# Kernel optimization log

Hardware: AMD Instinct MI355X
Metric: run time of the kernel (lower is better)

The kernel has to match this reference:

```python
import jax, jax.numpy as jnp
import numpy as np

N_NODES = 50000
N_EDGES = 1600000
IN_C, HID_C, OUT_C = 256, 256, 10


def setup_inputs() -> dict:
    key = jax.random.key(0)
    ks = jax.random.split(key, 8)
    x = jax.random.normal(ks[0], (N_NODES, IN_C), dtype=jnp.float32)
    edge_index = jax.random.randint(ks[1], (2, N_EDGES), 0, N_NODES, dtype=jnp.int64)
    s1 = 1.0 / np.sqrt(IN_C)
    s2 = 1.0 / np.sqrt(HID_C)
    W1l = jax.random.normal(ks[2], (IN_C, HID_C), dtype=jnp.float32) * s1
    W1r = jax.random.normal(ks[3], (IN_C, HID_C), dtype=jnp.float32) * s1
    b1 = jnp.zeros((HID_C,), dtype=jnp.float32)
    W2l = jax.random.normal(ks[4], (HID_C, OUT_C), dtype=jnp.float32) * s2
    W2r = jax.random.normal(ks[5], (HID_C, OUT_C), dtype=jnp.float32) * s2
    b2 = jnp.zeros((OUT_C,), dtype=jnp.float32)
    return {"x": x, "edge_index": edge_index, "W1l": W1l, "W1r": W1r,
            "b1": b1, "W2l": W2l, "W2r": W2r, "b2": b2}


def _mean_agg(x, src, dst, n):
    # scatter-mean of source features into destination nodes
    summed = jax.ops.segment_sum(x[src], dst, num_segments=n)  # [N, C]
    cnt = jax.ops.segment_sum(jnp.ones_like(dst, dtype=x.dtype), dst, num_segments=n)
    return summed / jnp.maximum(cnt, 1.0)[:, None]


def _sage_conv(x, src, dst, Wl, Wr, b):
    # PyG SAGEConv (mean aggr): lin_l(mean_j x_j) + lin_r(x_i) + bias
    n = x.shape[0]
    agg = _mean_agg(x, src, dst, n)
    return agg @ Wl + x @ Wr + b


def reference(x, edge_index, W1l, W1r, b1, W2l, W2r, b2):
    src = edge_index[0]
    dst = edge_index[1]
    h = _sage_conv(x, src, dst, W1l, W1r, b1)
    h = jax.nn.relu(h)  # dropout skipped: eval mode
    out = _sage_conv(h, src, dst, W2l, W2r, b2)
    return jax.nn.log_softmax(out, axis=1)
```

## Files before the change

kernel.cpp:

```cpp
#include <hip/hip_runtime.h>
#include <hip/hip_bf16.h>

#define N_NODES 50000
#define N_EDGES 1600000
#define IN_C 256
#define HID_C 256
#define OUT_C 10
#define SLOT_CAP 96
#define NBUCKET 196
#define CAP2 56
#define M_TILES 391
#define PART_BLOCKS 391
#define GEMM_BLOCKS 1568
#define PREP_BLOCKS 533

typedef short bf16x8 __attribute__((ext_vector_type(8)));
typedef float f32x4 __attribute__((ext_vector_type(4)));

static __device__ __forceinline__ float b2f(short v) {
    unsigned u = (unsigned)(unsigned short)v << 16;
    return __builtin_bit_cast(float, u);
}
static __device__ __forceinline__ short f2b(float f) {
    __hip_bfloat16 h = __float2bfloat16(f);
    return __builtin_bit_cast(short, h);
}
static __device__ __forceinline__ int4 pack8i(float4 a, float4 b) {
    bf16x8 o;
    o[0] = f2b(a.x); o[1] = f2b(a.y); o[2] = f2b(a.z); o[3] = f2b(a.w);
    o[4] = f2b(b.x); o[5] = f2b(b.y); o[6] = f2b(b.z); o[7] = f2b(b.w);
    return __builtin_bit_cast(int4, o);
}

__global__ void k_prep(const float* __restrict__ W1l, const float* __restrict__ W1r,
                       const float* __restrict__ W2l, const float* __restrict__ W2r,
                       __hip_bfloat16* __restrict__ Wt, float* __restrict__ Wt2f,
                       int* __restrict__ part_done) {
    int bid = blockIdx.x;
    if (bid < 512) {
        int idx = bid * 256 + threadIdx.x;
        int n = idx >> 8, k = idx & 255;
        float v = (n < HID_C) ? W1l[k * HID_C + n] : W1r[k * HID_C + (n - HID_C)];
        Wt[idx] = __float2bfloat16(v);
    } else if (bid < 532) {
        int idx = (bid - 512) * 256 + threadIdx.x;
        int r = idx >> 8, k = idx & 255;
        if (r < OUT_C) Wt2f[r * 256 + k] = W2l[k * OUT_C + r];
        else           Wt2f[(16 + r - OUT_C) * 256 + k] = W2r[k * OUT_C + (r - OUT_C)];
    } else {
        if (threadIdx.x == 0) *part_done = 0;
    }
}

__global__ __launch_bounds__(256) void k_gpb(
        const int* __restrict__ src, const int* __restrict__ dst,
        int* __restrict__ part_done, int* __restrict__ ebuf2,
        unsigned char* __restrict__ cnt2,
        int* __restrict__ cnt, unsigned short* __restrict__ slots,
        const float* __restrict__ X, const __hip_bfloat16* __restrict__ Wt,
        const float* __restrict__ b1,
        __hip_bfloat16* __restrict__ Ab, __hip_bfloat16* __restrict__ Bh) {
    __shared__ short Smem[2 * 128 * 64];
    int tid = threadIdx.x;

    if (blockIdx.x < PART_BLOCKS) {
        int* pos = (int*)Smem;
        int pb = blockIdx.x;
        if (tid < NBUCKET) pos[tid] = 0;
        __syncthreads();

        int4 s[4], d[4];
        bool valid[4];
#pragma unroll
        for (int q = 0; q < 4; ++q) {
            int idx = pb * 1024 + q * 256 + tid;
            valid[q] = (idx < N_EDGES / 4);
            if (valid[q]) {
                s[q] = ((const int4*)src)[idx];
                d[q] = ((const int4*)dst)[idx];
            }
        }
#pragma unroll
        for (int q = 0; q < 4; ++q) {
            if (valid[q]) {
                int ss[4] = { s[q].x, s[q].y, s[q].z, s[q].w };
                int dd[4] = { d[q].x, d[q].y, d[q].z, d[q].w };
#pragma unroll
                for (int e = 0; e < 4; ++e) {
                    int b = dd[e] >> 8;
                    int p = atomicAdd(&pos[b], 1);
                    if (p < CAP2)
                        ebuf2[((size_t)pb * NBUCKET + b) * CAP2 + p] =
                            ss[e] | ((dd[e] & 255) << 16);
                }
            }
        }
        __syncthreads();
        if (tid < NBUCKET) {
            int c = pos[tid];
            cnt2[(size_t)pb * NBUCKET + tid] = (unsigned char)(c > CAP2 ? CAP2 : c);
        }
        __syncthreads();
        if (tid == 0)
            __hip_atomic_fetch_add(part_done, 1, __ATOMIC_RELEASE, __HIP_MEMORY_SCOPE_AGENT);
        return;
    }

    if (blockIdx.x >= PART_BLOCKS + GEMM_BLOCKS) {
        if (tid == 0) {
            while (__hip_atomic_load(part_done, __ATOMIC_RELAXED,
                                     __HIP_MEMORY_SCOPE_AGENT) < PART_BLOCKS)
                __builtin_amdgcn_s_sleep(8);
        }
        __syncthreads();
        asm volatile("" ::: "memory");

        int* lcnt = (int*)Smem;
        int b = blockIdx.x - PART_BLOCKS - GEMM_BLOCKS;
        lcnt[tid] = 0;
        __syncthreads();
        for (int blk = tid; blk < PART_BLOCKS; blk += 256) {
            int len = cnt2[(size_t)blk * NBUCKET + b];
            const int* base2 = ebuf2 + ((size_t)blk * NBUCKET + b) * CAP2;
            for (int i = 0; i < len; ++i) {
                int rec = base2[i];
                int dl = (rec >> 16) & 255;
                int p = atomicAdd(&lcnt[dl], 1);
                if (p < SLOT_CAP)
                    slots[(size_t)(b * 256 + dl) * SLOT_CAP + p] = (unsigned short)(rec & 0xFFFF);
            }
        }
        __syncthreads();
        int nid = b * 256 + tid;
        if (nid < N_NODES) cnt[nid] = lcnt[tid];
        return;
    }

    short* As = Smem;
    short* Bs = Smem + 128 * 64;
    int fid = blockIdx.x - PART_BLOCKS;
    int xcd = fid & 7, slot = fid >> 3;
    int m_t = (slot >> 2) * 8 + xcd;
    if (m_t >= M_TILES) return;
    int n_t = slot & 3;
    int m_base = m_t * 128;
    int n_base = n_t * 128;

    int wave = tid >> 6, lane = tid & 63;
    int r = lane & 15, quad = lane >> 4;
    int wr = wave >> 1, wc = wave & 1;

    int srow = tid >> 3;
    int kb8  = (tid & 7) * 16;
    int kelem = (tid & 7) * 8;
    int swz  = kb8 ^ ((srow & 7) << 4);

    f32x4 acc[4][4];
#pragma unroll
    for (int i = 0; i < 4; ++i)
#pragma unroll
        for (int j = 0; j < 4; ++j) acc[i][j] = f32x4{0.f, 0.f, 0.f, 0.f};

    int4 av[4], bv[4];
#pragma unroll
    for (int q = 0; q < 4; ++q) {
        int grow = m_base + q * 32 + srow;
        if (grow > N_NODES - 1) grow = N_NODES - 1;
        const float* xp = X + (size_t)grow * IN_C + kelem;
        av[q] = pack8i(*(const float4*)xp, *(const float4*)(xp + 4));
        int brow = n_base + q * 32 + srow;
        bv[q] = *(const int4*)((const char*)Wt + ((size_t)brow * 512 + kb8));
    }

    for (int kk = 0; kk < 4; ++kk) {
        if (kk) __syncthreads();
#pragma unroll
        for (int q = 0; q < 4; ++q) {
            *(int4*)((char*)As + (size_t)((q * 32 + srow) * 128 + swz)) = av[q];
            *(int4*)((char*)Bs + (size_t)((q * 32 + srow) * 128 + swz)) = bv[q];
        }
        __syncthreads();

        if (kk < 3) {
            int ke = (kk + 1) * 64 + kelem;
            int kbyte = (kk + 1) * 128 + kb8;
#pragma unroll
            for (int q = 0; q < 4; ++q) {
                int grow = m_base + q * 32 + srow;
                if (grow > N_NODES - 1) grow = N_NODES - 1;
                const float* xp = X + (size_t)grow * IN_C + ke;
                av[q] = pack8i(*(const float4*)xp, *(const float4*)(xp + 4));
                int brow = n_base + q * 32 + srow;
                bv[q] = *(const int4*)((const char*)Wt + ((size_t)brow * 512 + kbyte));
            }
        }

#pragma unroll
        for (int s = 0; s < 2; ++s) {
            int kfb = (s * 64 + quad * 16) ^ ((r & 7) << 4);
            bf16x8 a[4], b[4];
#pragma unroll
            for (int i = 0; i < 4; ++i)
                a[i] = *(const bf16x8*)((const char*)As + (size_t)((wr * 64 + i * 16 + r) * 128) + kfb);
#pragma unroll
            for (int j = 0; j < 4; ++j)
                b[j] = *(const bf16x8*)((const char*)Bs + (size_t)((wc * 64 + j * 16 + r) * 128) + kfb);
#pragma unroll
            for (int i = 0; i < 4; ++i)
#pragma unroll
                for (int j = 0; j < 4; ++j)
                    acc[i][j] = __builtin_amdgcn_mfma_f32_16x16x32_bf16(a[i], b[j], acc[i][j], 0, 0, 0);
        }
    }

    __syncthreads();
    short* Cs = Smem;
    bool left = (n_base < HID_C);
#pragma unroll
    for (int j = 0; j < 4; ++j) {
        int coll = wc * 64 + 16 * j + r;
        float bias = left ? 0.f : b1[n_base + coll - HID_C];
#pragma unroll
        for (int i = 0; i < 4; ++i) {
#pragma unroll
            for (int ii = 0; ii < 4; ++ii) {
                int rowl = wr * 64 + 16 * i + quad * 4 + ii;
                int byteoff = (coll * 2) ^ ((rowl & 7) << 4);
                *(short*)((char*)Cs + rowl * 256 + byteoff) = f2b(acc[i][j][ii] + bias);
            }
        }
    }
    __syncthreads();

    int rrow = tid >> 4;
    int cchunk = (tid & 15) * 16;
    size_t colbyte = left ? (size_t)(n_base * 2) : (size_t)((n_base - HID_C) * 2);
    char* outp = left ? (char*)Ab : (char*)Bh;
    for (int rb = 0; rb < 128; rb += 16) {
        int rowl = rb + rrow;
        int4 v = *(const int4*)((const char*)Cs + rowl * 256 + (cchunk ^ ((rowl & 7) << 4)));
        int grow = m_base + rowl;
        if (grow < N_NODES)
            *(int4*)(outp + (size_t)grow * 512 + colbyte + cchunk) = v;
    }
}

__global__ __launch_bounds__(256) void k_agg1f(
        const __hip_bfloat16* __restrict__ Ab, const __hip_bfloat16* __restrict__ Bh,
        const int* __restrict__ cnt, const unsigned short* __restrict__ slots,
        const float* __restrict__ Wt2f, const float* __restrict__ b2,
        float* __restrict__ CDl, float* __restrict__ CDr) {
    int wave = threadIdx.x >> 6, lane = threadIdx.x & 63;
    int nid = blockIdx.x * 4 + wave;
    int half = lane >> 5;
    int c8 = (lane & 31) * 8;
    const unsigned short* row = slots + (size_t)nid * SLOT_CAP;
    int n = cnt[nid];
    if (n > SLOT_CAP) n = SLOT_CAP;
    int mid = (n + 1) >> 1;
    int beg = half ? mid : 0;
    int end = half ? n : mid;

    float s0[8], s1[8], s2[8], s3[8];
#pragma unroll
    for (int j = 0; j < 8; ++j) { s0[j] = 0.f; s1[j] = 0.f; s2[j] = 0.f; s3[j] = 0.f; }

    const __hip_bfloat16* abc = Ab + c8;
    int e = beg;
    for (; e + 4 <= end; e += 4) {
        int i0 = row[e], i1 = row[e + 1], i2 = row[e + 2], i3 = row[e + 3];
        bf16x8 v0 = *(const bf16x8*)(abc + (size_t)i0 * HID_C);
        bf16x8 v1 = *(const bf16x8*)(abc + (size_t)i1 * HID_C);
        bf16x8 v2 = *(const bf16x8*)(abc + (size_t)i2 * HID_C);
        bf16x8 v3 = *(const bf16x8*)(abc + (size_t)i3 * HID_C);
#pragma unroll
        for (int j = 0; j < 8; ++j) {
            s0[j] += b2f(v0[j]); s1[j] += b2f(v1[j]);
            s2[j] += b2f(v2[j]); s3[j] += b2f(v3[j]);
        }
    }
    for (; e < end; ++e) {
        int i0 = row[e];
        bf16x8 v0 = *(const bf16x8*)(abc + (size_t)i0 * HID_C);
#pragma unroll
        for (int j = 0; j < 8; ++j) s0[j] += b2f(v0[j]);
    }
#pragma unroll
    for (int j = 0; j < 8; ++j) s0[j] += (s1[j] + s2[j]) + s3[j];
#pragma unroll
    for (int j = 0; j < 8; ++j) s0[j] += __shfl_down(s0[j], 32, 64);

    float h[8];
    float inv = 1.f / fmaxf((float)n, 1.f);
    if (half == 0) {
        bf16x8 bb = *(const bf16x8*)(Bh + (size_t)nid * HID_C + c8);
#pragma unroll
        for (int j = 0; j < 8; ++j)
            h[j] = fmaxf(s0[j] * inv + b2f(bb[j]), 0.f);
    }
#pragma unroll
    for (int j = 0; j < 8; ++j) h[j] = __shfl(h[j], lane & 31, 64);

    const float* wbase = Wt2f + (half ? 16 * 256 : 0);
    float acc[10];
#pragma unroll
    for (int j = 0; j < 10; ++j) {
        f32x4 w0 = *(const f32x4*)(wbase + j * 256 + c8);
        f32x4 w1 = *(const f32x4*)(wbase + j * 256 + c8 + 4);
        float a = h[0] * w0[0] + h[1] * w0[1] + h[2] * w0[2] + h[3] * w0[3]
                + h[4] * w1[0] + h[5] * w1[1] + h[6] * w1[2] + h[7] * w1[3];
#pragma unroll
        for (int off = 16; off > 0; off >>= 1)
            a += __shfl_down(a, off, 32);
        acc[j] = a;
    }
    if ((lane & 31) == 0) {
        if (half == 0) {
            float* o = CDl + (size_t)nid * 12;
#pragma unroll
            for (int j = 0; j < 10; ++j) o[j] = acc[j];
            o[10] = 0.f; o[11] = 0.f;
        } else {
            float* o = CDr + (size_t)nid * 12;
#pragma unroll
            for (int j = 0; j < 10; ++j) o[j] = acc[j] + b2[j];
        }
    }
}

__global__ __launch_bounds__(256) void k_agg2(
        const float* __restrict__ CDl, const float* __restrict__ CDr,
        const int* __restrict__ cnt, const unsigned short* __restrict__ slots,
        float* __restrict__ out) {
    int wave = threadIdx.x >> 6, lane = threadIdx.x & 63;
    int half = lane >> 5, sub = lane & 31;
    int nid = blockIdx.x * 8 + wave * 2 + half;
    const unsigned short* row = slots + (size_t)nid * SLOT_CAP;
    int n = cnt[nid];
    if (n > SLOT_CAP) n = SLOT_CAP;
    float s[10];
#pragma unroll
    for (int j = 0; j < 10; ++j) s[j] = 0.f;
    for (int e = sub; e < n; e += 32) {
        const float* cr = CDl + (size_t)row[e] * 12;
        f32x4 v0 = *(const f32x4*)cr;
        f32x4 v1 = *(const f32x4*)(cr + 4);
        f32x4 v2 = *(const f32x4*)(cr + 8);
#pragma unroll
        for (int j = 0; j < 4; ++j) { s[j] += v0[j]; s[4 + j] += v1[j]; }
        s[8] += v2[0]; s[9] += v2[1];
    }
#pragma unroll
    for (int j = 0; j < 10; ++j)
#pragma unroll
        for (int off = 16; off > 0; off >>= 1)
            s[j] += __shfl_down(s[j], off, 32);
    if (sub == 0) {
        float inv = 1.f / fmaxf((float)n, 1.f);
        const float* rr = CDr + (size_t)nid * 12;
        float z[10], mx = -1e30f;
#pragma unroll
        for (int j = 0; j < 10; ++j) {
            z[j] = s[j] * inv + rr[j];
            mx = fmaxf(mx, z[j]);
        }
        float se = 0.f;
#pragma unroll
        for (int j = 0; j < 10; ++j) se += expf(z[j] - mx);
        float lse = logf(se) + mx;
#pragma unroll
        for (int j = 0; j < 10; ++j) out[(size_t)nid * OUT_C + j] = z[j] - lse;
    }
}

extern "C" void kernel_launch(void* const* d_in, const int* in_sizes, int n_in,
                              void* d_out, int out_size, void* d_ws, size_t ws_size,
                              hipStream_t stream) {
    const float* x   = (const float*)d_in[0];
    const int*   ei  = (const int*)d_in[1];
    const float* W1l = (const float*)d_in[2];
    const float* W1r = (const float*)d_in[3];
    const float* b1  = (const float*)d_in[4];
    const float* W2l = (const float*)d_in[5];
    const float* W2r = (const float*)d_in[6];
    const float* b2  = (const float*)d_in[7];
    float* out = (float*)d_out;
    const int* src = ei;
    const int* dst = ei + N_EDGES;

    char* w = (char*)d_ws;
    size_t off = 0;
    auto alloc = [&](size_t bytes) -> void* {
        void* p = w + off;
        off = (off + bytes + 255) & ~(size_t)255;
        return p;
    };
    __hip_bfloat16* Wt   = (__hip_bfloat16*)alloc((size_t)2 * HID_C * IN_C * 2);
    float*          Wt2f = (float*)alloc((size_t)32 * 256 * 4);
    __hip_bfloat16* Ab   = (__hip_bfloat16*)alloc((size_t)N_NODES * HID_C * 2);
    __hip_bfloat16* Bh   = (__hip_bfloat16*)alloc((size_t)N_NODES * HID_C * 2);
    float* CDl = (float*)alloc((size_t)N_NODES * 12 * 4);
    float* CDr = (float*)alloc((size_t)N_NODES * 12 * 4);
    int* cnt      = (int*)alloc((size_t)N_NODES * 4);
    unsigned short* slots = (unsigned short*)alloc((size_t)N_NODES * SLOT_CAP * 2);
    int* part_done = (int*)alloc(4);
    int* ebuf2     = (int*)alloc((size_t)PART_BLOCKS * NBUCKET * CAP2 * 4);
    unsigned char* cnt2 = (unsigned char*)alloc((size_t)PART_BLOCKS * NBUCKET);

    k_prep<<<PREP_BLOCKS, 256, 0, stream>>>(W1l, W1r, W2l, W2r, Wt, Wt2f, part_done);
    k_gpb<<<PART_BLOCKS + GEMM_BLOCKS + NBUCKET, 256, 0, stream>>>(
        src, dst, part_done, ebuf2, cnt2, cnt, slots, x, Wt, b1, Ab, Bh);
    k_agg1f<<<N_NODES / 4, 256, 0, stream>>>(Ab, Bh, cnt, slots, Wt2f, b2, CDl, CDr);
    k_agg2<<<N_NODES / 8, 256, 0, stream>>>(CDl, CDr, cnt, slots, out);
}
```

Baseline: 339.6 us.

## Move edge partitioning into prep kernel and drop spin-wait flag

Edge partitioning moves from the fused GEMM/bucket kernel into the weight-prep kernel. Bucket-fill blocks now run first in the second kernel and no longer spin-wait on an atomic completion counter, because the kernel boundary orders them after partitioning. This removes the spin-wait and the flag reset. The cost is that partitioning no longer overlaps with the layer-1 GEMM blocks, so partition work sits on the critical path before the GEMM starts.

Result: faster. 320.2 us (-5.7%).

```diff
diff --git a/kernel.cpp b/kernel.cpp
--- a/kernel.cpp
+++ b/kernel.cpp
@@ -12,7 +12,7 @@
 #define M_TILES 391
 #define PART_BLOCKS 391
 #define GEMM_BLOCKS 1568
-#define PREP_BLOCKS 533
+#define PREP_BLOCKS 532
 
 typedef short bf16x8 __attribute__((ext_vector_type(8)));
 typedef float f32x4 __attribute__((ext_vector_type(4)));
@@ -32,30 +32,70 @@
     return __builtin_bit_cast(int4, o);
 }
 
-__global__ void k_prep(const float* __restrict__ W1l, const float* __restrict__ W1r,
-                       const float* __restrict__ W2l, const float* __restrict__ W2r,
-                       __hip_bfloat16* __restrict__ Wt, float* __restrict__ Wt2f,
-                       int* __restrict__ part_done) {
+__global__ __launch_bounds__(256) void k_pp(
+        const float* __restrict__ W1l, const float* __restrict__ W1r,
+        const float* __restrict__ W2l, const float* __restrict__ W2r,
+        __hip_bfloat16* __restrict__ Wt, float* __restrict__ Wt2f,
+        const int* __restrict__ src, const int* __restrict__ dst,
+        int* __restrict__ ebuf2, unsigned char* __restrict__ cnt2) {
+    __shared__ int pos[NBUCKET];
+    int tid = threadIdx.x;
     int bid = blockIdx.x;
+
     if (bid < 512) {
-        int idx = bid * 256 + threadIdx.x;
+        int idx = bid * 256 + tid;
         int n = idx >> 8, k = idx & 255;
         float v = (n < HID_C) ? W1l[k * HID_C + n] : W1r[k * HID_C + (n - HID_C)];
         Wt[idx] = __float2bfloat16(v);
-    } else if (bid < 532) {
-        int idx = (bid - 512) * 256 + threadIdx.x;
+        return;
+    }
+    if (bid < PREP_BLOCKS) {
+        int idx = (bid - 512) * 256 + tid;
         int r = idx >> 8, k = idx & 255;
         if (r < OUT_C) Wt2f[r * 256 + k] = W2l[k * OUT_C + r];
         else           Wt2f[(16 + r - OUT_C) * 256 + k] = W2r[k * OUT_C + (r - OUT_C)];
-    } else {
-        if (threadIdx.x == 0) *part_done = 0;
-    }
-}
-
-__global__ __launch_bounds__(256) void k_gpb(
-        const int* __restrict__ src, const int* __restrict__ dst,
-        int* __restrict__ part_done, int* __restrict__ ebuf2,
-        unsigned char* __restrict__ cnt2,
+        return;
+    }
+
+    int pb = bid - PREP_BLOCKS;
+    if (tid < NBUCKET) pos[tid] = 0;
+    __syncthreads();
+
+    int4 s[4], d[4];
+    bool valid[4];
+#pragma unroll
+    for (int q = 0; q < 4; ++q) {
+        int idx = pb * 1024 + q * 256 + tid;
+        valid[q] = (idx < N_EDGES / 4);
+        if (valid[q]) {
+            s[q] = ((const int4*)src)[idx];
+            d[q] = ((const int4*)dst)[idx];
+        }
+    }
+#pragma unroll
+    for (int q = 0; q < 4; ++q) {
+        if (valid[q]) {
+            int ss[4] = { s[q].x, s[q].y, s[q].z, s[q].w };
+            int dd[4] = { d[q].x, d[q].y, d[q].z, d[q].w };
+#pragma unroll
+            for (int e = 0; e < 4; ++e) {
+                int b = dd[e] >> 8;
+                int p = atomicAdd(&pos[b], 1);
+                if (p < CAP2)
+                    ebuf2[((size_t)pb * NBUCKET + b) * CAP2 + p] =
+                        ss[e] | ((dd[e] & 255) << 16);
+            }
+        }
+    }
+    __syncthreads();
+    if (tid < NBUCKET) {
+        int c = pos[tid];
+        cnt2[(size_t)pb * NBUCKET + tid] = (unsigned char)(c > CAP2 ? CAP2 : c);
+    }
+}
+
+__global__ __launch_bounds__(256) void k_gb(
+        const int* __restrict__ ebuf2, const unsigned char* __restrict__ cnt2,
         int* __restrict__ cnt, unsigned short* __restrict__ slots,
         const float* __restrict__ X, const __hip_bfloat16* __restrict__ Wt,
         const float* __restrict__ b1,
@@ -63,60 +103,9 @@
     __shared__ short Smem[2 * 128 * 64];
     int tid = threadIdx.x;
 
-    if (blockIdx.x < PART_BLOCKS) {
-        int* pos = (int*)Smem;
-        int pb = blockIdx.x;
-        if (tid < NBUCKET) pos[tid] = 0;
-        __syncthreads();
-
-        int4 s[4], d[4];
-        bool valid[4];
-#pragma unroll
-        for (int q = 0; q < 4; ++q) {
-            int idx = pb * 1024 + q * 256 + tid;
-            valid[q] = (idx < N_EDGES / 4);
-            if (valid[q]) {
-                s[q] = ((const int4*)src)[idx];
-                d[q] = ((const int4*)dst)[idx];
-            }
-        }
-#pragma unroll
-        for (int q = 0; q < 4; ++q) {
-            if (valid[q]) {
-                int ss[4] = { s[q].x, s[q].y, s[q].z, s[q].w };
-                int dd[4] = { d[q].x, d[q].y, d[q].z, d[q].w };
-#pragma unroll
-                for (int e = 0; e < 4; ++e) {
-                    int b = dd[e] >> 8;
-                    int p = atomicAdd(&pos[b], 1);
-                    if (p < CAP2)
-                        ebuf2[((size_t)pb * NBUCKET + b) * CAP2 + p] =
-                            ss[e] | ((dd[e] & 255) << 16);
-                }
-            }
-        }
-        __syncthreads();
-        if (tid < NBUCKET) {
-            int c = pos[tid];
-            cnt2[(size_t)pb * NBUCKET + tid] = (unsigned char)(c > CAP2 ? CAP2 : c);
-        }
-        __syncthreads();
-        if (tid == 0)
-            __hip_atomic_fetch_add(part_done, 1, __ATOMIC_RELEASE, __HIP_MEMORY_SCOPE_AGENT);
-        return;
-    }
-
-    if (blockIdx.x >= PART_BLOCKS + GEMM_BLOCKS) {
-        if (tid == 0) {
-            while (__hip_atomic_load(part_done, __ATOMIC_RELAXED,
-                                     __HIP_MEMORY_SCOPE_AGENT) < PART_BLOCKS)
-                __builtin_amdgcn_s_sleep(8);
-        }
-        __syncthreads();
-        asm volatile("" ::: "memory");
-
+    if (blockIdx.x < NBUCKET) {
         int* lcnt = (int*)Smem;
-        int b = blockIdx.x - PART_BLOCKS - GEMM_BLOCKS;
+        int b = blockIdx.x;
         lcnt[tid] = 0;
         __syncthreads();
         for (int blk = tid; blk < PART_BLOCKS; blk += 256) {
@@ -138,7 +127,7 @@
 
     short* As = Smem;
     short* Bs = Smem + 128 * 64;
-    int fid = blockIdx.x - PART_BLOCKS;
+    int fid = blockIdx.x - NBUCKET;
     int xcd = fid & 7, slot = fid >> 3;
     int m_t = (slot >> 2) * 8 + xcd;
     if (m_t >= M_TILES) return;
@@ -403,13 +392,13 @@
     float* CDr = (float*)alloc((size_t)N_NODES * 12 * 4);
     int* cnt      = (int*)alloc((size_t)N_NODES * 4);
     unsigned short* slots = (unsigned short*)alloc((size_t)N_NODES * SLOT_CAP * 2);
-    int* part_done = (int*)alloc(4);
     int* ebuf2     = (int*)alloc((size_t)PART_BLOCKS * NBUCKET * CAP2 * 4);
     unsigned char* cnt2 = (unsigned char*)alloc((size_t)PART_BLOCKS * NBUCKET);
 
-    k_prep<<<PREP_BLOCKS, 256, 0, stream>>>(W1l, W1r, W2l, W2r, Wt, Wt2f, part_done);
-    k_gpb<<<PART_BLOCKS + GEMM_BLOCKS + NBUCKET, 256, 0, stream>>>(
-        src, dst, part_done, ebuf2, cnt2, cnt, slots, x, Wt, b1, Ab, Bh);
+    k_pp<<<PREP_BLOCKS + PART_BLOCKS, 256, 0, stream>>>(W1l, W1r, W2l, W2r, Wt, Wt2f,
+                                                        src, dst, ebuf2, cnt2);
+    k_gb<<<NBUCKET + GEMM_BLOCKS, 256, 0, stream>>>(ebuf2, cnt2, cnt, slots,
+                                                    x, Wt, b1, Ab, Bh);
     k_agg1f<<<N_NODES / 4, 256, 0, stream>>>(Ab, Bh, cnt, slots, Wt2f, b2, CDl, CDr);
     k_agg2<<<N_NODES / 8, 256, 0, stream>>>(CDl, CDr, cnt, slots, out);
 }
```
